# Kernel tuning notes

Hardware: AMD Instinct MI355X
Metric: run time of the kernel (lower is better)

## Reference

```python
import jax, jax.numpy as jnp
import numpy as np

B, N, IN, H = 8, 2048, 256, 128
ALPHA = 0.2  # leaky relu slope


def setup_inputs() -> dict:
    key = jax.random.key(0)
    k1, k2, k3, k4 = jax.random.split(key, 4)
    x = jax.random.normal(k1, (B, N, IN), dtype=jnp.float32)
    # adj_identity: batched identity matrix (masks self-attention, then re-adds weight-1 self loop)
    adj_identity = jnp.broadcast_to(jnp.eye(N, dtype=jnp.float32), (B, N, N))
    W = jax.random.normal(k2, (H, IN), dtype=jnp.float32) * (1.0 / np.sqrt(IN))
    b = jnp.zeros((H,), dtype=jnp.float32)
    # atten_fact: [2H, 1], xavier_normal with gain=1.414
    std = 1.414 * np.sqrt(2.0 / (2 * H + 1))
    a = jax.random.normal(k3, (2 * H, 1), dtype=jnp.float32) * std
    return {"input": x, "adj_identity": adj_identity, "W": W, "b": b, "a": a}


def reference(input, adj_identity, W, b, a):
    # input projection: [B,N,H]
    h = jnp.einsum("bni,hi->bnh", input, W) + b
    # decomposition of cat([h_i, h_j]) @ a == h_i@a1 + h_j@a2 (exact same math,
    # avoids materializing the [B, N*N, 2H] tensor)
    a1 = a[:H, 0]  # [H]
    a2 = a[H:, 0]  # [H]
    si = h @ a1  # [B,N]
    sj = h @ a2  # [B,N]
    scores = jax.nn.leaky_relu(si[:, :, None] + sj[:, None, :], negative_slope=ALPHA)  # [B,N,N]
    scores = jnp.where(adj_identity != 0, -jnp.inf, scores)
    attn = jax.nn.softmax(scores, axis=-1) + adj_identity  # [B,N,N]
    # dropout p=0.0 -> identity
    out = jax.nn.elu(jnp.einsum("bnm,bmh->bnh", attn, h))
    return out
```

## Files before the change

kernel.cpp:

```cpp
#include <hip/hip_runtime.h>
#include <hip/hip_bf16.h>
#include <cmath>


#define ALPHA 0.2f
#define NN 2048
#define NIN 256
#define NH 128

typedef __attribute__((ext_vector_type(8))) short short8;
typedef __attribute__((ext_vector_type(4))) float f32x4;

__device__ __forceinline__ unsigned short f2bf(float f) {
    unsigned int u = __float_as_uint(f);
    u += 0x7fffu + ((u >> 16) & 1u);
    return (unsigned short)(u >> 16);
}

__global__ __launch_bounds__(256) void k1_h(
    const float* __restrict__ x, const float* __restrict__ Wm,
    const float* __restrict__ bias, const float* __restrict__ av,
    float* __restrict__ hout, float* __restrict__ si, float* __restrict__ sj,
    unsigned short* __restrict__ hTt)
{
    __shared__ __align__(16) unsigned short xls[64 * 264];
    __shared__ __align__(16) unsigned short Wls[128 * 264];
    __shared__ float a1l[128], a2l[128], bl[128];

    const int t = threadIdx.x;
    const int r0 = blockIdx.x * 64;

    for (int p = 0; p < 16; ++p) {
        int idx = p * 256 + t;
        int row = idx >> 6, kq = idx & 63;
        f32x4 v = *(const f32x4*)(x + (size_t)(r0 + row) * NIN + kq * 4);
        unsigned int lo = (unsigned)f2bf(v[0]) | ((unsigned)f2bf(v[1]) << 16);
        unsigned int hi = (unsigned)f2bf(v[2]) | ((unsigned)f2bf(v[3]) << 16);
        *(uint2*)(&xls[row * 264 + kq * 4]) = make_uint2(lo, hi);
    }
    for (int p = 0; p < 32; ++p) {
        int idx = p * 256 + t;
        int row = idx >> 6, kq = idx & 63;
        f32x4 v = *(const f32x4*)(Wm + (size_t)row * NIN + kq * 4);
        unsigned int lo = (unsigned)f2bf(v[0]) | ((unsigned)f2bf(v[1]) << 16);
        unsigned int hi = (unsigned)f2bf(v[2]) | ((unsigned)f2bf(v[3]) << 16);
        *(uint2*)(&Wls[row * 264 + kq * 4]) = make_uint2(lo, hi);
    }
    if (t < 128) { a1l[t] = av[t]; a2l[t] = av[128 + t]; bl[t] = bias[t]; }
    __syncthreads();

    const int w = t >> 6, l = t & 63, la = l & 15, g = l >> 4;

    f32x4 acc[8];
#pragma unroll
    for (int n = 0; n < 8; ++n) acc[n] = (f32x4){0.f, 0.f, 0.f, 0.f};

#pragma unroll
    for (int ks = 0; ks < 8; ++ks) {
        short8 af = *(const short8*)(&xls[(w * 16 + la) * 264 + ks * 32 + g * 8]);
#pragma unroll
        for (int n = 0; n < 8; ++n) {
            short8 bfr = *(const short8*)(&Wls[(n * 16 + la) * 264 + ks * 32 + g * 8]);
            acc[n] = __builtin_amdgcn_mfma_f32_16x16x32_bf16(af, bfr, acc[n], 0, 0, 0);
        }
    }

    float s1[4] = {0.f, 0.f, 0.f, 0.f}, s2[4] = {0.f, 0.f, 0.f, 0.f};
#pragma unroll
    for (int n = 0; n < 8; ++n) {
        int col = n * 16 + la;
#pragma unroll
        for (int r = 0; r < 4; ++r) {
            float v = acc[n][r] + bl[col];
            acc[n][r] = v;
            int row = w * 16 + g * 4 + r;
            hout[(size_t)(r0 + row) * NH + col] = v;
            s1[r] += v * a1l[col];
            s2[r] += v * a2l[col];
        }
    }
#pragma unroll
    for (int r = 0; r < 4; ++r) {
#pragma unroll
        for (int m = 1; m < 16; m <<= 1) {
            s1[r] += __shfl_xor(s1[r], m, 64);
            s2[r] += __shfl_xor(s2[r], m, 64);
        }
    }
    if (la == 0) {
#pragma unroll
        for (int r = 0; r < 4; ++r) {
            int row = w * 16 + g * 4 + r;
            si[r0 + row] = s1[r];
            sj[r0 + row] = s2[r];
        }
    }

    __syncthreads();
    unsigned short* oT = xls;
#pragma unroll
    for (int n = 0; n < 8; ++n) {
        int col = n * 16 + la;
        int row0 = w * 16 + g * 4;
        unsigned int lo = (unsigned)f2bf(acc[n][0]) | ((unsigned)f2bf(acc[n][1]) << 16);
        unsigned int hi = (unsigned)f2bf(acc[n][2]) | ((unsigned)f2bf(acc[n][3]) << 16);
        *(uint2*)(&oT[col * 72 + row0]) = make_uint2(lo, hi);
    }
    __syncthreads();
    const int b = r0 >> 11, jt = (r0 & (NN - 1)) >> 6;
    unsigned short* dst = hTt + ((size_t)(b * 32 + jt)) * 8192;
    for (int p = 0; p < 4; ++p) {
        int idx = p * 256 + t;
        int col = idx >> 3, seg = idx & 7;
        uint4 v = *(const uint4*)(&oT[col * 72 + seg * 8]);
        *(uint4*)(dst + col * 64 + seg * 8) = v;
    }
}

__global__ __launch_bounds__(512) void k3_attn(
    const float* __restrict__ h, const unsigned short* __restrict__ hTt,
    const float* __restrict__ si, const float* __restrict__ sj,
    float* __restrict__ out)
{
    __shared__ __align__(16) float f1l[NN];
    __shared__ __align__(16) float f2l[NN];
    __shared__ __align__(16) unsigned short hl[2][128 * 72];
    __shared__ float Zl[64];
    __shared__ float mr1[8], mr2[8];

    const int t = threadIdx.x;
    const int bb = blockIdx.x >> 5;
    const int i0 = (blockIdx.x & 31) * 64;
    const int w = t >> 6, l = t & 63;
    const int wr = w >> 1, wc = w & 1;
    const int la = l & 15, g = l >> 4;

    const unsigned short* tb = hTt + (size_t)bb * 32 * 8192;

    uint4 c0 = ((const uint4*)tb)[t];
    uint4 c1 = ((const uint4*)tb)[t + 512];

    ((f32x4*)f1l)[t] = ((const f32x4*)(sj + bb * NN))[t];
    __syncthreads();
    float vv[4];
    {
        f32x4 r = ((const f32x4*)f1l)[t];
        vv[0] = r[0]; vv[1] = r[1]; vv[2] = r[2]; vv[3] = r[3];
    }
    float m1 = fmaxf(fmaxf(vv[0], vv[1]), fmaxf(vv[2], vv[3]));
    float m2 = fminf(fmaxf(fmaxf(vv[0], vv[1]), fminf(vv[2], vv[3])),
                     fmaxf(fminf(vv[0], vv[1]), fmaxf(vv[2], vv[3])));
    m2 = fmaxf(m2, fminf(fmaxf(vv[0], vv[2]), fmaxf(vv[1], vv[3])));
    {
        float a = vv[0], b2 = vv[1];
        float hi0 = fmaxf(a, b2), lo0 = fminf(a, b2);
        float hi1 = fmaxf(vv[2], vv[3]), lo1 = fminf(vv[2], vv[3]);
        m1 = fmaxf(hi0, hi1);
        m2 = fmaxf(fminf(hi0, hi1), fmaxf(lo0, lo1));
    }
#pragma unroll
    for (int m = 1; m < 64; m <<= 1) {
        float o1 = __shfl_xor(m1, m, 64), o2 = __shfl_xor(m2, m, 64);
        float n1 = fmaxf(m1, o1);
        float n2 = fmaxf(fminf(m1, o1), fmaxf(m2, o2));
        m1 = n1; m2 = n2;
    }
    if (l == 0) { mr1[w] = m1; mr2[w] = m2; }
    __syncthreads();
    {
        float a1 = mr1[0], a2 = mr2[0];
#pragma unroll
        for (int wv = 1; wv < 8; ++wv) {
            float b1 = mr1[wv], b2 = mr2[wv];
            float n1 = fmaxf(a1, b1), n2 = fmaxf(fminf(a1, b1), fmaxf(a2, b2));
            a1 = n1; a2 = n2;
        }
        m1 = a1; m2 = a2;
    }
    {
        f32x4 e1v, e2v;
#pragma unroll
        for (int u = 0; u < 4; ++u) { e1v[u] = expf(vv[u]); e2v[u] = expf(ALPHA * vv[u]); }
        ((f32x4*)f1l)[t] = e1v;
        ((f32x4*)f2l)[t] = e2v;
    }

    const int irow = i0 + wr * 16 + la;
    const int gibase = bb * NN + irow;
    const float svi = si[gibase];
    const float svjo = sj[gibase];
    float e1, e2, T, ow;
    {
        float M = (svjo == m1) ? m2 : m1;
        float sm = svi + M;
        float m = sm > 0.f ? sm : ALPHA * sm;
        e1 = expf(svi - m);
        e2 = expf(ALPHA * svi - m);
        T  = expf(-svi);
        float sd = svi + svjo;
        float lr = sd > 0.f ? sd : ALPHA * sd;
        ow = expf(lr - m);
    }

    f32x4 acc[4];
#pragma unroll
    for (int n = 0; n < 4; ++n) acc[n] = (f32x4){0.f, 0.f, 0.f, 0.f};
    float z = 0.f;

    const int sidx0 = (t >> 3) * 72 + (t & 7) * 8;
    const int sidx1 = ((t + 512) >> 3) * 72 + (t & 7) * 8;

    for (int jt = 0; jt < 32; ++jt) {
        unsigned short* buf = hl[jt & 1];
        *(uint4*)(&buf[sidx0]) = c0;
        *(uint4*)(&buf[sidx1]) = c1;
        if (jt < 31) {
            const uint4* nt = (const uint4*)(tb + (size_t)(jt + 1) * 8192);
            c0 = nt[t];
            c1 = nt[t + 512];
        }
        __syncthreads();

        const int j0 = jt * 64;
#pragma unroll
        for (int ks = 0; ks < 2; ++ks) {
            const int jb = j0 + ks * 32 + g * 8;
            f32x4 F1a = *(const f32x4*)(f1l + jb);
            f32x4 F1b = *(const f32x4*)(f1l + jb + 4);
            f32x4 F2a = *(const f32x4*)(f2l + jb);
            f32x4 F2b = *(const f32x4*)(f2l + jb + 4);
            short8 af;
#pragma unroll
            for (int u = 0; u < 4; ++u) {
                {
                    float fa = F1a[u], fb = F2a[u];
                    bool c = fa > T;
                    float wv = (c ? e1 : e2) * (c ? fa : fb);
                    z += wv;
                    af[u] = (short)f2bf(wv);
                }
                {
                    float fa = F1b[u], fb = F2b[u];
                    bool c = fa > T;
                    float wv = (c ? e1 : e2) * (c ? fa : fb);
                    z += wv;
                    af[u + 4] = (short)f2bf(wv);
                }
            }
#pragma unroll
            for (int n = 0; n < 4; ++n) {
                int col = wc * 64 + n * 16 + la;
                short8 bfr = *(const short8*)(&buf[col * 72 + ks * 32 + g * 8]);
                acc[n] = __builtin_amdgcn_mfma_f32_16x16x32_bf16(af, bfr, acc[n], 0, 0, 0);
            }
        }
    }

    z += __shfl_xor(z, 16, 64);
    z += __shfl_xor(z, 32, 64);
    if (wc == 0) Zl[wr * 16 + la] = z;
    __syncthreads();

#pragma unroll
    for (int n = 0; n < 4; ++n) {
        int col = wc * 64 + n * 16 + la;
#pragma unroll
        for (int r = 0; r < 4; ++r) {
            int row = wr * 16 + g * 4 + r;
            int gi = bb * NN + i0 + row;
            float Z  = Zl[row];
            float owr = (row == (wr * 16 + la)) ? ow : 0.f;
            (void)owr;
            float hv = h[(size_t)gi * NH + col];
            int srcl = (row & 15) | (l & 48);
            float e1r = __shfl(e1, srcl, 64);
            float e2r = __shfl(e2, srcl, 64);
            float owq = __shfl(ow, srcl, 64);
            float ZT  = Z;
            float s1v = acc[n][r];
            float num = s1v - owq * hv;
            float den = ZT - owq;
            float o = num / den + hv;
            out[(size_t)gi * NH + col] = o > 0.f ? o : expm1f(o);
            (void)e1r; (void)e2r;
        }
    }
}

extern "C" void kernel_launch(void* const* d_in, const int* in_sizes, int n_in,
                              void* d_out, int out_size, void* d_ws, size_t ws_size,
                              hipStream_t stream)
{
    const float* x    = (const float*)d_in[0];
    const float* Wm   = (const float*)d_in[2];
    const float* bias = (const float*)d_in[3];
    const float* av   = (const float*)d_in[4];
    float* out = (float*)d_out;

    float* wsf = (float*)d_ws;
    float* h   = wsf;
    float* si  = wsf + 2097152;
    float* sj  = wsf + 2113536;
    unsigned short* hTt = (unsigned short*)(wsf + 2129920);

    hipLaunchKernelGGL(k1_h,    dim3(256), dim3(256), 0, stream, x, Wm, bias, av, h, si, sj, hTt);
    hipLaunchKernelGGL(k3_attn, dim3(256), dim3(512), 0, stream, h, hTt, si, sj, out);
}
```

Measured before the change: 50.14 us.

## Restructure attention kernel: split-K waves, MFMA row sums, drop fp32 h buffer

Replaces the software bf16 rounding with the hardware packed convert instruction. Stops writing the fp32 h tensor and reads the self-loop term from the bf16 transposed copy instead. Changes the wave layout so each wave computes two row fragments over half of K, with a cross-wave reduction through LDS. The branchy weight selection becomes a branch-free max of two products, and the softmax denominator is now computed by an MFMA against a vector of ones. This cuts global traffic and VALU work per tile, but the h term in the output now comes from bf16 values and there is extra reduction and synchronisation overhead at the end.

```diff
diff --git a/kernel.cpp b/kernel.cpp
--- a/kernel.cpp
+++ b/kernel.cpp
@@ -11,16 +11,16 @@
 typedef __attribute__((ext_vector_type(8))) short short8;
 typedef __attribute__((ext_vector_type(4))) float f32x4;
 
-__device__ __forceinline__ unsigned short f2bf(float f) {
-    unsigned int u = __float_as_uint(f);
-    u += 0x7fffu + ((u >> 16) & 1u);
-    return (unsigned short)(u >> 16);
+__device__ __forceinline__ unsigned int pk2(float a, float b) {
+    unsigned int r;
+    asm("v_cvt_pk_bf16_f32 %0, %1, %2" : "=v"(r) : "v"(a), "v"(b));
+    return r;
 }
 
 __global__ __launch_bounds__(256) void k1_h(
     const float* __restrict__ x, const float* __restrict__ Wm,
     const float* __restrict__ bias, const float* __restrict__ av,
-    float* __restrict__ hout, float* __restrict__ si, float* __restrict__ sj,
+    float* __restrict__ si, float* __restrict__ sj,
     unsigned short* __restrict__ hTt)
 {
     __shared__ __align__(16) unsigned short xls[64 * 264];
@@ -34,17 +34,13 @@
         int idx = p * 256 + t;
         int row = idx >> 6, kq = idx & 63;
         f32x4 v = *(const f32x4*)(x + (size_t)(r0 + row) * NIN + kq * 4);
-        unsigned int lo = (unsigned)f2bf(v[0]) | ((unsigned)f2bf(v[1]) << 16);
-        unsigned int hi = (unsigned)f2bf(v[2]) | ((unsigned)f2bf(v[3]) << 16);
-        *(uint2*)(&xls[row * 264 + kq * 4]) = make_uint2(lo, hi);
+        *(uint2*)(&xls[row * 264 + kq * 4]) = make_uint2(pk2(v[0], v[1]), pk2(v[2], v[3]));
     }
     for (int p = 0; p < 32; ++p) {
         int idx = p * 256 + t;
         int row = idx >> 6, kq = idx & 63;
         f32x4 v = *(const f32x4*)(Wm + (size_t)row * NIN + kq * 4);
-        unsigned int lo = (unsigned)f2bf(v[0]) | ((unsigned)f2bf(v[1]) << 16);
-        unsigned int hi = (unsigned)f2bf(v[2]) | ((unsigned)f2bf(v[3]) << 16);
-        *(uint2*)(&Wls[row * 264 + kq * 4]) = make_uint2(lo, hi);
+        *(uint2*)(&Wls[row * 264 + kq * 4]) = make_uint2(pk2(v[0], v[1]), pk2(v[2], v[3]));
     }
     if (t < 128) { a1l[t] = av[t]; a2l[t] = av[128 + t]; bl[t] = bias[t]; }
     __syncthreads();
@@ -73,8 +69,6 @@
         for (int r = 0; r < 4; ++r) {
             float v = acc[n][r] + bl[col];
             acc[n][r] = v;
-            int row = w * 16 + g * 4 + r;
-            hout[(size_t)(r0 + row) * NH + col] = v;
             s1[r] += v * a1l[col];
             s2[r] += v * a2l[col];
         }
@@ -102,9 +96,8 @@
     for (int n = 0; n < 8; ++n) {
         int col = n * 16 + la;
         int row0 = w * 16 + g * 4;
-        unsigned int lo = (unsigned)f2bf(acc[n][0]) | ((unsigned)f2bf(acc[n][1]) << 16);
-        unsigned int hi = (unsigned)f2bf(acc[n][2]) | ((unsigned)f2bf(acc[n][3]) << 16);
-        *(uint2*)(&oT[col * 72 + row0]) = make_uint2(lo, hi);
+        *(uint2*)(&oT[col * 72 + row0]) =
+            make_uint2(pk2(acc[n][0], acc[n][1]), pk2(acc[n][2], acc[n][3]));
     }
     __syncthreads();
     const int b = r0 >> 11, jt = (r0 & (NN - 1)) >> 6;
@@ -118,42 +111,36 @@
 }
 
 __global__ __launch_bounds__(512) void k3_attn(
-    const float* __restrict__ h, const unsigned short* __restrict__ hTt,
+    const unsigned short* __restrict__ hTt,
     const float* __restrict__ si, const float* __restrict__ sj,
     float* __restrict__ out)
 {
     __shared__ __align__(16) float f1l[NN];
     __shared__ __align__(16) float f2l[NN];
     __shared__ __align__(16) unsigned short hl[2][128 * 72];
-    __shared__ float Zl[64];
+    __shared__ float Zl[2][64];
     __shared__ float mr1[8], mr2[8];
 
     const int t = threadIdx.x;
     const int bb = blockIdx.x >> 5;
     const int i0 = (blockIdx.x & 31) * 64;
     const int w = t >> 6, l = t & 63;
-    const int wr = w >> 1, wc = w & 1;
+    const int wr = w >> 2;
+    const int wcg = (w >> 1) & 1;
+    const int wk = w & 1;
     const int la = l & 15, g = l >> 4;
 
-    const unsigned short* tb = hTt + (size_t)bb * 32 * 8192;
+    const unsigned short* tb = hTt + (size_t)bb * (32 * 8192);
 
     uint4 c0 = ((const uint4*)tb)[t];
     uint4 c1 = ((const uint4*)tb)[t + 512];
 
     ((f32x4*)f1l)[t] = ((const f32x4*)(sj + bb * NN))[t];
     __syncthreads();
-    float vv[4];
+    f32x4 vv = ((const f32x4*)f1l)[t];
+    float m1, m2;
     {
-        f32x4 r = ((const f32x4*)f1l)[t];
-        vv[0] = r[0]; vv[1] = r[1]; vv[2] = r[2]; vv[3] = r[3];
-    }
-    float m1 = fmaxf(fmaxf(vv[0], vv[1]), fmaxf(vv[2], vv[3]));
-    float m2 = fminf(fmaxf(fmaxf(vv[0], vv[1]), fminf(vv[2], vv[3])),
-                     fmaxf(fminf(vv[0], vv[1]), fmaxf(vv[2], vv[3])));
-    m2 = fmaxf(m2, fminf(fmaxf(vv[0], vv[2]), fmaxf(vv[1], vv[3])));
-    {
-        float a = vv[0], b2 = vv[1];
-        float hi0 = fmaxf(a, b2), lo0 = fminf(a, b2);
+        float hi0 = fmaxf(vv[0], vv[1]), lo0 = fminf(vv[0], vv[1]);
         float hi1 = fmaxf(vv[2], vv[3]), lo1 = fminf(vv[2], vv[3]);
         m1 = fmaxf(hi0, hi1);
         m2 = fmaxf(fminf(hi0, hi1), fmaxf(lo0, lo1));
@@ -170,42 +157,45 @@
     {
         float a1 = mr1[0], a2 = mr2[0];
 #pragma unroll
-        for (int wv = 1; wv < 8; ++wv) {
-            float b1 = mr1[wv], b2 = mr2[wv];
+        for (int wv2 = 1; wv2 < 8; ++wv2) {
+            float b1 = mr1[wv2], b2 = mr2[wv2];
             float n1 = fmaxf(a1, b1), n2 = fmaxf(fminf(a1, b1), fmaxf(a2, b2));
             a1 = n1; a2 = n2;
         }
         m1 = a1; m2 = a2;
     }
     {
-        f32x4 e1v, e2v;
-#pragma unroll
-        for (int u = 0; u < 4; ++u) { e1v[u] = expf(vv[u]); e2v[u] = expf(ALPHA * vv[u]); }
-        ((f32x4*)f1l)[t] = e1v;
-        ((f32x4*)f2l)[t] = e2v;
-    }
-
-    const int irow = i0 + wr * 16 + la;
-    const int gibase = bb * NN + irow;
-    const float svi = si[gibase];
-    const float svjo = sj[gibase];
-    float e1, e2, T, ow;
-    {
-        float M = (svjo == m1) ? m2 : m1;
+        f32x4 e1t, e2t;
+#pragma unroll
+        for (int u = 0; u < 4; ++u) { e1t[u] = expf(vv[u]); e2t[u] = expf(ALPHA * vv[u]); }
+        ((f32x4*)f1l)[t] = e1t;
+        ((f32x4*)f2l)[t] = e2t;
+    }
+
+    float e1v[2], e2v[2], owv[2];
+#pragma unroll
+    for (int fr = 0; fr < 2; ++fr) {
+        int gi = bb * NN + i0 + wr * 32 + fr * 16 + la;
+        float svi = si[gi], svj = sj[gi];
+        float M = (svj == m1) ? m2 : m1;
         float sm = svi + M;
-        float m = sm > 0.f ? sm : ALPHA * sm;
-        e1 = expf(svi - m);
-        e2 = expf(ALPHA * svi - m);
-        T  = expf(-svi);
-        float sd = svi + svjo;
-        float lr = sd > 0.f ? sd : ALPHA * sd;
-        ow = expf(lr - m);
-    }
-
-    f32x4 acc[4];
-#pragma unroll
-    for (int n = 0; n < 4; ++n) acc[n] = (f32x4){0.f, 0.f, 0.f, 0.f};
-    float z = 0.f;
+        float mm = sm > 0.f ? sm : ALPHA * sm;
+        float a = expf(svi - mm), b2 = expf(ALPHA * svi - mm);
+        e1v[fr] = a; e2v[fr] = b2;
+        float owr = fmaxf(a * expf(svj), b2 * expf(ALPHA * svj));
+        owv[fr] = __uint_as_float(pk2(owr, owr) << 16);
+    }
+
+    f32x4 acc[2][4], zac[2];
+#pragma unroll
+    for (int fr = 0; fr < 2; ++fr) {
+        zac[fr] = (f32x4){0.f, 0.f, 0.f, 0.f};
+#pragma unroll
+        for (int n = 0; n < 4; ++n) acc[fr][n] = (f32x4){0.f, 0.f, 0.f, 0.f};
+    }
+    short8 ones;
+#pragma unroll
+    for (int u = 0; u < 8; ++u) ones[u] = (short)0x3F80;
 
     const int sidx0 = (t >> 3) * 72 + (t & 7) * 8;
     const int sidx1 = ((t + 512) >> 3) * 72 + (t & 7) * 8;
@@ -221,68 +211,91 @@
         }
         __syncthreads();
 
-        const int j0 = jt * 64;
-#pragma unroll
-        for (int ks = 0; ks < 2; ++ks) {
-            const int jb = j0 + ks * 32 + g * 8;
-            f32x4 F1a = *(const f32x4*)(f1l + jb);
-            f32x4 F1b = *(const f32x4*)(f1l + jb + 4);
-            f32x4 F2a = *(const f32x4*)(f2l + jb);
-            f32x4 F2b = *(const f32x4*)(f2l + jb + 4);
-            short8 af;
-#pragma unroll
-            for (int u = 0; u < 4; ++u) {
-                {
-                    float fa = F1a[u], fb = F2a[u];
-                    bool c = fa > T;
-                    float wv = (c ? e1 : e2) * (c ? fa : fb);
-                    z += wv;
-                    af[u] = (short)f2bf(wv);
-                }
-                {
-                    float fa = F1b[u], fb = F2b[u];
-                    bool c = fa > T;
-                    float wv = (c ? e1 : e2) * (c ? fa : fb);
-                    z += wv;
-                    af[u + 4] = (short)f2bf(wv);
+        const int jb = jt * 64 + wk * 32 + g * 8;
+        f32x4 F1a = *(const f32x4*)(f1l + jb);
+        f32x4 F1b = *(const f32x4*)(f1l + jb + 4);
+        f32x4 F2a = *(const f32x4*)(f2l + jb);
+        f32x4 F2b = *(const f32x4*)(f2l + jb + 4);
+
+        short8 af[2];
+#pragma unroll
+        for (int fr = 0; fr < 2; ++fr) {
+            const float e1 = e1v[fr], e2 = e2v[fr];
+            float w0 = fmaxf(e1 * F1a[0], e2 * F2a[0]);
+            float w1 = fmaxf(e1 * F1a[1], e2 * F2a[1]);
+            float w2 = fmaxf(e1 * F1a[2], e2 * F2a[2]);
+            float w3 = fmaxf(e1 * F1a[3], e2 * F2a[3]);
+            float w4 = fmaxf(e1 * F1b[0], e2 * F2b[0]);
+            float w5 = fmaxf(e1 * F1b[1], e2 * F2b[1]);
+            float w6 = fmaxf(e1 * F1b[2], e2 * F2b[2]);
+            float w7 = fmaxf(e1 * F1b[3], e2 * F2b[3]);
+            union { unsigned int u[4]; short8 s; } cv;
+            cv.u[0] = pk2(w0, w1);
+            cv.u[1] = pk2(w2, w3);
+            cv.u[2] = pk2(w4, w5);
+            cv.u[3] = pk2(w6, w7);
+            af[fr] = cv.s;
+        }
+#pragma unroll
+        for (int n = 0; n < 4; ++n) {
+            const int col = wcg * 64 + n * 16 + la;
+            short8 bfr = *(const short8*)(&buf[col * 72 + wk * 32 + g * 8]);
+            acc[0][n] = __builtin_amdgcn_mfma_f32_16x16x32_bf16(af[0], bfr, acc[0][n], 0, 0, 0);
+            acc[1][n] = __builtin_amdgcn_mfma_f32_16x16x32_bf16(af[1], bfr, acc[1][n], 0, 0, 0);
+        }
+        zac[0] = __builtin_amdgcn_mfma_f32_16x16x32_bf16(af[0], ones, zac[0], 0, 0, 0);
+        zac[1] = __builtin_amdgcn_mfma_f32_16x16x32_bf16(af[1], ones, zac[1], 0, 0, 0);
+    }
+
+    __syncthreads();
+    float* xch = (float*)hl;
+    const int pair = wr * 2 + wcg;
+    if (wk == 1) {
+#pragma unroll
+        for (int fr = 0; fr < 2; ++fr)
+#pragma unroll
+            for (int n = 0; n < 4; ++n)
+#pragma unroll
+                for (int r = 0; r < 4; ++r)
+                    xch[(fr * 16 + n * 4 + r) * 256 + pair * 64 + l] = acc[fr][n][r];
+    }
+    if (wcg == 0 && la == 0) {
+#pragma unroll
+        for (int fr = 0; fr < 2; ++fr)
+#pragma unroll
+            for (int r = 0; r < 4; ++r)
+                Zl[wk][wr * 32 + fr * 16 + g * 4 + r] = zac[fr][r];
+    }
+    __syncthreads();
+
+    if (wk == 0) {
+#pragma unroll
+        for (int fr = 0; fr < 2; ++fr)
+#pragma unroll
+            for (int n = 0; n < 4; ++n)
+#pragma unroll
+                for (int r = 0; r < 4; ++r)
+                    acc[fr][n][r] += xch[(fr * 16 + n * 4 + r) * 256 + pair * 64 + l];
+
+#pragma unroll
+        for (int fr = 0; fr < 2; ++fr) {
+#pragma unroll
+            for (int n = 0; n < 4; ++n) {
+                const int col = wcg * 64 + n * 16 + la;
+#pragma unroll
+                for (int r = 0; r < 4; ++r) {
+                    const int row = wr * 32 + fr * 16 + g * 4 + r;
+                    const float Z = Zl[0][row] + Zl[1][row];
+                    const int srcl = (g * 4 + r) | (l & 48);
+                    const float owq = __shfl(owv[fr], srcl, 64);
+                    const float hv = __uint_as_float(
+                        (unsigned int)tb[(i0 >> 6) * 8192 + col * 64 + row] << 16);
+                    const float num = acc[fr][n][r] - owq * hv;
+                    const float den = Z - owq;
+                    float o = num / den + hv;
+                    out[(size_t)(bb * NN + i0 + row) * NH + col] = o > 0.f ? o : expm1f(o);
                 }
             }
-#pragma unroll
-            for (int n = 0; n < 4; ++n) {
-                int col = wc * 64 + n * 16 + la;
-                short8 bfr = *(const short8*)(&buf[col * 72 + ks * 32 + g * 8]);
-                acc[n] = __builtin_amdgcn_mfma_f32_16x16x32_bf16(af, bfr, acc[n], 0, 0, 0);
-            }
-        }
-    }
-
-    z += __shfl_xor(z, 16, 64);
-    z += __shfl_xor(z, 32, 64);
-    if (wc == 0) Zl[wr * 16 + la] = z;
-    __syncthreads();
-
-#pragma unroll
-    for (int n = 0; n < 4; ++n) {
-        int col = wc * 64 + n * 16 + la;
-#pragma unroll
-        for (int r = 0; r < 4; ++r) {
-            int row = wr * 16 + g * 4 + r;
-            int gi = bb * NN + i0 + row;
-            float Z  = Zl[row];
-            float owr = (row == (wr * 16 + la)) ? ow : 0.f;
-            (void)owr;
-            float hv = h[(size_t)gi * NH + col];
-            int srcl = (row & 15) | (l & 48);
-            float e1r = __shfl(e1, srcl, 64);
-            float e2r = __shfl(e2, srcl, 64);
-            float owq = __shfl(ow, srcl, 64);
-            float ZT  = Z;
-            float s1v = acc[n][r];
-            float num = s1v - owq * hv;
-            float den = ZT - owq;
-            float o = num / den + hv;
-            out[(size_t)gi * NH + col] = o > 0.f ? o : expm1f(o);
-            (void)e1r; (void)e2r;
         }
     }
 }
@@ -298,11 +311,10 @@
     float* out = (float*)d_out;
 
     float* wsf = (float*)d_ws;
-    float* h   = wsf;
-    float* si  = wsf + 2097152;
-    float* sj  = wsf + 2113536;
-    unsigned short* hTt = (unsigned short*)(wsf + 2129920);
-
-    hipLaunchKernelGGL(k1_h,    dim3(256), dim3(256), 0, stream, x, Wm, bias, av, h, si, sj, hTt);
-    hipLaunchKernelGGL(k3_attn, dim3(256), dim3(512), 0, stream, h, hTt, si, sj, out);
+    unsigned short* hTt = (unsigned short*)wsf;
+    float* si = wsf + 1048576;
+    float* sj = wsf + 1064960;
+
+    hipLaunchKernelGGL(k1_h,    dim3(256), dim3(256), 0, stream, x, Wm, bias, av, si, sj, hTt);
+    hipLaunchKernelGGL(k3_attn, dim3(256), dim3(512), 0, stream, hTt, si, sj, out);
 }
```

Result: faster. 42.31 us (-15.6%).
